# Optimization experiments

Hardware: AMD Instinct MI355X
Metric: run time of the kernel (lower is better)

Reference implementation:

```python
import jax, jax.numpy as jnp
import numpy as np

T_LATENCY = 2  # refractory latency (timesteps), from init_kwargs
FS_SCALE = 10.0  # FastSigmoid surrogate scale


@jax.custom_vjp
def fast_sigmoid_spike(u):
    return (u > 0).astype(u.dtype)

def _fs_fwd(u):
    return fast_sigmoid_spike(u), u

def _fs_bwd(u, g):
    return (g / (FS_SCALE * jnp.abs(u) + 1.0) ** 2,)

fast_sigmoid_spike.defvjp(_fs_fwd, _fs_bwd)


def setup_inputs() -> dict:
    key = jax.random.key(0)
    k1, k2, k3, k4 = jax.random.split(key, 4)
    B, N, T = 64, 1024, 512
    x = jax.random.normal(k1, (B, N, T), dtype=jnp.float32)
    beta = jax.random.uniform(k2, (N,), jnp.float32, 0.3, 0.95)   # leak
    p = jax.random.uniform(k3, (N,), jnp.float32, 0.5, 0.95)      # adaptation decay
    b = jax.random.uniform(k4, (N,), jnp.float32, 0.5, 1.5)       # adaptation strength
    return {"x": x, "beta": beta, "p": p, "b": b}


def reference(x, beta, p, b):
    # clamped effective params (matches torch @property accessors)
    beta_c = jnp.clip(beta, 0.001, 0.999)
    p_c = jnp.clip(jnp.abs(p), 0.0, 0.999)
    b_c = jnp.clip(jnp.abs(b), 0.001, 1.0)

    B, N, T = x.shape
    xt = jnp.moveaxis(x, 2, 0)  # [T, B, N]

    def step(carry, x_t):
        mem, spikes, refac, a, v_th = carry
        # spike-triggered refractory reset, then mask input during refractory window
        refac = jnp.where(spikes > 0, 0.0, refac)
        ic = jnp.where(refac < T_LATENCY, 0.0, x_t)
        refac = refac + 1.0
        # leaky integration
        new_mem = mem * beta_c + ic
        s = fast_sigmoid_spike(new_mem - v_th)
        # reset-by-subtraction-to-zero with detached spikes (detach_spike_grad=True)
        mem = new_mem * (1.0 - jax.lax.stop_gradient(s))
        # adaptive threshold
        a = p_c * a + s
        v_th = 1.0 + b_c * a
        return (mem, s, refac, a, v_th), s

    z = jnp.zeros((B, N), x.dtype)
    init = (z, z, jnp.full((B, N), float(T_LATENCY), x.dtype), z,
            jnp.ones((B, N), x.dtype))
    _, spikes_seq = jax.lax.scan(step, init, xt)  # [T, B, N]
    return jnp.moveaxis(spikes_seq, 0, 2)  # [B, N, T]
```

## Files before the change

kernel.cpp:

```cpp
#include <hip/hip_runtime.h>

#pragma clang fp contract(off)

#define ROWS    64
#define T_LEN   512
#define CHUNK   64
#define NCHUNK  (T_LEN / CHUNK)
#define NV      16
#define BUFW    (ROWS * CHUNK)
#define NPARAM  1024

typedef float f4_nt __attribute__((ext_vector_type(4)));

#define BARRIER() asm volatile("s_waitcnt lgkmcnt(0)\n\ts_barrier" ::: "memory")

#define GLOAD16(gp, lp)                                                \
    __builtin_amdgcn_global_load_lds(                                  \
        (const __attribute__((address_space(1))) void*)(gp),           \
        (__attribute__((address_space(3))) void*)(lp), 16, 0, 0)

__global__ __launch_bounds__(128) void snn_fwd(
    const float* __restrict__ x,
    const float* __restrict__ beta,
    const float* __restrict__ p,
    const float* __restrict__ bparam,
    float* __restrict__ out)
{
    __shared__ __align__(16) float inbuf[3][BUFW];
    __shared__ __align__(16) unsigned int bitlds[ROWS][16];

    const int tid     = threadIdx.x;
    const int wid     = tid >> 6;
    const int lane    = tid & 63;
    const int rowBase = blockIdx.x * ROWS;

    const float4* __restrict__ xv = (const float4*)x;
    float4* __restrict__ ov       = (float4*)out;

    const int t16 = lane & 15;
    const int r4  = lane >> 4;
    const int gEven = (rowBase + r4) * (T_LEN / 4) + (t16 ^ r4);
    const int gOdd  = gEven ^ 4;

    float mem = 0.0f, refac = 2.0f, a = 0.0f, vth = 1.0f, ps = 0.0f;
    float beta_c = 0.f, p_c = 0.f, b_c = 0.f;
    const int swl   = (lane & 3) | (((lane >> 2) & 1) << 2);
    const int cbase = lane * NV;

    if (wid == 0) {
        const int n = (rowBase + lane) & (NPARAM - 1);
        beta_c = fminf(fmaxf(beta[n], 0.001f), 0.999f);
        p_c    = fminf(fabsf(p[n]), 0.999f);
        b_c    = fminf(fmaxf(fabsf(bparam[n]), 0.001f), 1.0f);
    }

    unsigned int b0 = 0, b1 = 0;

    auto step = [&](float xt, unsigned int msk, unsigned int& bw) {
        refac = (ps > 0.0f) ? 0.0f : refac;
        const float ic = (refac < 2.0f) ? 0.0f : xt;
        refac += 1.0f;
        const float nm   = __fadd_rn(__fmul_rn(mem, beta_c), ic);
        const float diff = __fsub_rn(nm, vth);
        const bool  sp   = diff > 0.0f;
        const float s    = sp ? 1.0f : 0.0f;
        bw |= sp ? msk : 0u;
        mem = sp ? 0.0f : nm;
        a   = __fadd_rn(__fmul_rn(p_c, a), s);
        vth = __fadd_rn(1.0f, __fmul_rn(b_c, a));
        ps  = s;
    };

    auto issue = [&](int c, int buf) {
        float* lb = &inbuf[buf][0];
        #pragma unroll
        for (int it = 0; it < NV; ++it) {
            const int gidx = ((it & 1) ? gOdd : gEven)
                           + it * 4 * (T_LEN / 4) + c * NV;
            GLOAD16(&xv[gidx], lb + it * 256);
        }
    };

    if (wid == 1) {
        issue(0, 0);
        issue(1, 1);
        asm volatile("s_waitcnt vmcnt(16)" ::: "memory");
    }
    BARRIER();

    int km3 = 0;
    #pragma unroll 1
    for (int k = 0; k < NCHUNK; ++k) {
        if (wid == 0) {
            b0 = 0; b1 = 0;
            const float4* ib = (const float4*)inbuf[km3];
            #pragma unroll
            for (int g = 0; g < NV; ++g) {
                const float4 v = ib[cbase + (g ^ swl)];
                const int t = 4 * g;
                if (t < 32) {
                    step(v.x, 1u << (t + 0), b0);
                    step(v.y, 1u << (t + 1), b0);
                    step(v.z, 1u << (t + 2), b0);
                    step(v.w, 1u << (t + 3), b0);
                } else {
                    step(v.x, 1u << (t - 32), b1);
                    step(v.y, 1u << (t - 31), b1);
                    step(v.z, 1u << (t - 30), b1);
                    step(v.w, 1u << (t - 29), b1);
                }
            }
            *(uint2*)&bitlds[lane][2 * k] = make_uint2(b0, b1);
        } else {
            if (k + 2 < NCHUNK) {
                int nb = km3 + 2; if (nb >= 3) nb -= 3;
                issue(k + 2, nb);
            }
            if (k < NCHUNK - 2)
                asm volatile("s_waitcnt vmcnt(16)" ::: "memory");
            else if (k == NCHUNK - 2)
                asm volatile("s_waitcnt vmcnt(0)" ::: "memory");
        }
        BARRIER();
        ++km3; if (km3 == 3) km3 = 0;
    }

    const int obase = rowBase * (T_LEN / 4);
    #pragma unroll 4
    for (int i = 0; i < ROWS; ++i) {
        const unsigned int w = bitlds[i][tid >> 3];
        const int s = (tid & 7) * 4;
        float4 sv;
        sv.x = (float)((w >> (s + 0)) & 1u);
        sv.y = (float)((w >> (s + 1)) & 1u);
        sv.z = (float)((w >> (s + 2)) & 1u);
        sv.w = (float)((w >> (s + 3)) & 1u);
        __builtin_nontemporal_store(
            *reinterpret_cast<f4_nt*>(&sv),
            reinterpret_cast<f4_nt*>(&ov[obase + i * 128 + tid]));
    }
}

extern "C" void kernel_launch(void* const* d_in, const int* in_sizes, int n_in,
                              void* d_out, int out_size, void* d_ws, size_t ws_size,
                              hipStream_t stream) {
    const float* x    = (const float*)d_in[0];
    const float* beta = (const float*)d_in[1];
    const float* p    = (const float*)d_in[2];
    const float* b    = (const float*)d_in[3];
    float* out        = (float*)d_out;

    const int BN = 64 * 1024;
    snn_fwd<<<dim3(BN / ROWS), dim3(128), 0, stream>>>(x, beta, p, b, out);
}
```

Measured before the change: 244.9 us.

## Use tiny one-wave blocks loading whole rows, computing in LDS with 16 lanes

Replaces the 64-row block, which had a producer wave and a triple-buffered chunk pipeline, with 64-thread blocks that each handle 16 rows. Each block loads its full 16x512 slab into LDS at once with direct global-to-LDS loads, and 16 lanes run the serial recurrence while writing spikes back in place. The result is then stored out. The block count goes up by 4x, so latency is hidden through many resident blocks rather than explicit pipelining. Only 16 of 64 lanes do the serial compute, and the bit-packing step is dropped.

Result: slower. 279.2 us (+14.0%).

```diff
diff --git a/kernel.cpp b/kernel.cpp
--- a/kernel.cpp
+++ b/kernel.cpp
@@ -2,61 +2,51 @@
 
 #pragma clang fp contract(off)
 
-#define ROWS    64
+#define ROWSB   16
 #define T_LEN   512
-#define CHUNK   64
-#define NCHUNK  (T_LEN / CHUNK)
-#define NV      16
-#define BUFW    (ROWS * CHUNK)
+#define QPR     128
 #define NPARAM  1024
 
 typedef float f4_nt __attribute__((ext_vector_type(4)));
-
-#define BARRIER() asm volatile("s_waitcnt lgkmcnt(0)\n\ts_barrier" ::: "memory")
 
 #define GLOAD16(gp, lp)                                                \
     __builtin_amdgcn_global_load_lds(                                  \
         (const __attribute__((address_space(1))) void*)(gp),           \
         (__attribute__((address_space(3))) void*)(lp), 16, 0, 0)
 
-__global__ __launch_bounds__(128) void snn_fwd(
+__global__ __launch_bounds__(64) void snn_fwd(
     const float* __restrict__ x,
     const float* __restrict__ beta,
     const float* __restrict__ p,
     const float* __restrict__ bparam,
     float* __restrict__ out)
 {
-    __shared__ __align__(16) float inbuf[3][BUFW];
-    __shared__ __align__(16) unsigned int bitlds[ROWS][16];
+    __shared__ __align__(16) float4 xbuf[ROWSB * QPR];
 
-    const int tid     = threadIdx.x;
-    const int wid     = tid >> 6;
-    const int lane    = tid & 63;
-    const int rowBase = blockIdx.x * ROWS;
+    const int lane    = threadIdx.x;
+    const int rowBase = blockIdx.x * ROWSB;
 
-    const float4* __restrict__ xv = (const float4*)x;
-    float4* __restrict__ ov       = (float4*)out;
+    const float4* __restrict__ xq = (const float4*)x + (size_t)rowBase * QPR;
+    float4* __restrict__ oq       = (float4*)out + (size_t)rowBase * QPR;
 
-    const int t16 = lane & 15;
-    const int r4  = lane >> 4;
-    const int gEven = (rowBase + r4) * (T_LEN / 4) + (t16 ^ r4);
-    const int gOdd  = gEven ^ 4;
+    #pragma unroll
+    for (int j = 0; j < 2 * ROWSB; ++j) {
+        const int L  = j >> 1;
+        const int qg = (((j & 1) << 6) | lane) ^ (L & 7);
+        GLOAD16(xq + L * QPR + qg, (float*)xbuf + j * 256);
+    }
 
-    float mem = 0.0f, refac = 2.0f, a = 0.0f, vth = 1.0f, ps = 0.0f;
-    float beta_c = 0.f, p_c = 0.f, b_c = 0.f;
-    const int swl   = (lane & 3) | (((lane >> 2) & 1) << 2);
-    const int cbase = lane * NV;
-
-    if (wid == 0) {
-        const int n = (rowBase + lane) & (NPARAM - 1);
+    float beta_c, p_c, b_c;
+    {
+        const int n = (rowBase + (lane & (ROWSB - 1))) & (NPARAM - 1);
         beta_c = fminf(fmaxf(beta[n], 0.001f), 0.999f);
         p_c    = fminf(fabsf(p[n]), 0.999f);
         b_c    = fminf(fmaxf(fabsf(bparam[n]), 0.001f), 1.0f);
     }
 
-    unsigned int b0 = 0, b1 = 0;
+    float mem = 0.0f, refac = 2.0f, a = 0.0f, vth = 1.0f, ps = 0.0f;
 
-    auto step = [&](float xt, unsigned int msk, unsigned int& bw) {
+    auto step = [&](float xt) -> float {
         refac = (ps > 0.0f) ? 0.0f : refac;
         const float ic = (refac < 2.0f) ? 0.0f : xt;
         refac += 1.0f;
@@ -64,80 +54,42 @@
         const float diff = __fsub_rn(nm, vth);
         const bool  sp   = diff > 0.0f;
         const float s    = sp ? 1.0f : 0.0f;
-        bw |= sp ? msk : 0u;
         mem = sp ? 0.0f : nm;
         a   = __fadd_rn(__fmul_rn(p_c, a), s);
         vth = __fadd_rn(1.0f, __fmul_rn(b_c, a));
         ps  = s;
+        return s;
     };
 
-    auto issue = [&](int c, int buf) {
-        float* lb = &inbuf[buf][0];
-        #pragma unroll
-        for (int it = 0; it < NV; ++it) {
-            const int gidx = ((it & 1) ? gOdd : gEven)
-                           + it * 4 * (T_LEN / 4) + c * NV;
-            GLOAD16(&xv[gidx], lb + it * 256);
+    asm volatile("s_waitcnt vmcnt(0)" ::: "memory");
+
+    if (lane < ROWSB) {
+        const int L7 = lane & 7;
+        float4* xb = xbuf + lane * QPR;
+        float4 p0 = xb[0 ^ L7];
+        float4 p1 = xb[1 ^ L7];
+        #pragma unroll 2
+        for (int t4 = 0; t4 < QPR; t4 += 2) {
+            float4 n0 = xb[((t4 + 2) & (QPR - 1)) ^ L7];
+            float4 s0;
+            s0.x = step(p0.x); s0.y = step(p0.y);
+            s0.z = step(p0.z); s0.w = step(p0.w);
+            xb[t4 ^ L7] = s0;
+            float4 n1 = xb[((t4 + 3) & (QPR - 1)) ^ L7];
+            float4 s1;
+            s1.x = step(p1.x); s1.y = step(p1.y);
+            s1.z = step(p1.z); s1.w = step(p1.w);
+            xb[(t4 + 1) ^ L7] = s1;
+            p0 = n0; p1 = n1;
         }
-    };
-
-    if (wid == 1) {
-        issue(0, 0);
-        issue(1, 1);
-        asm volatile("s_waitcnt vmcnt(16)" ::: "memory");
-    }
-    BARRIER();
-
-    int km3 = 0;
-    #pragma unroll 1
-    for (int k = 0; k < NCHUNK; ++k) {
-        if (wid == 0) {
-            b0 = 0; b1 = 0;
-            const float4* ib = (const float4*)inbuf[km3];
-            #pragma unroll
-            for (int g = 0; g < NV; ++g) {
-                const float4 v = ib[cbase + (g ^ swl)];
-                const int t = 4 * g;
-                if (t < 32) {
-                    step(v.x, 1u << (t + 0), b0);
-                    step(v.y, 1u << (t + 1), b0);
-                    step(v.z, 1u << (t + 2), b0);
-                    step(v.w, 1u << (t + 3), b0);
-                } else {
-                    step(v.x, 1u << (t - 32), b1);
-                    step(v.y, 1u << (t - 31), b1);
-                    step(v.z, 1u << (t - 30), b1);
-                    step(v.w, 1u << (t - 29), b1);
-                }
-            }
-            *(uint2*)&bitlds[lane][2 * k] = make_uint2(b0, b1);
-        } else {
-            if (k + 2 < NCHUNK) {
-                int nb = km3 + 2; if (nb >= 3) nb -= 3;
-                issue(k + 2, nb);
-            }
-            if (k < NCHUNK - 2)
-                asm volatile("s_waitcnt vmcnt(16)" ::: "memory");
-            else if (k == NCHUNK - 2)
-                asm volatile("s_waitcnt vmcnt(0)" ::: "memory");
-        }
-        BARRIER();
-        ++km3; if (km3 == 3) km3 = 0;
     }
 
-    const int obase = rowBase * (T_LEN / 4);
-    #pragma unroll 4
-    for (int i = 0; i < ROWS; ++i) {
-        const unsigned int w = bitlds[i][tid >> 3];
-        const int s = (tid & 7) * 4;
-        float4 sv;
-        sv.x = (float)((w >> (s + 0)) & 1u);
-        sv.y = (float)((w >> (s + 1)) & 1u);
-        sv.z = (float)((w >> (s + 2)) & 1u);
-        sv.w = (float)((w >> (s + 3)) & 1u);
+    #pragma unroll
+    for (int j = 0; j < 2 * ROWSB; ++j) {
+        const float4 sv = xbuf[j * 64 + (lane ^ ((j >> 1) & 7))];
         __builtin_nontemporal_store(
-            *reinterpret_cast<f4_nt*>(&sv),
-            reinterpret_cast<f4_nt*>(&ov[obase + i * 128 + tid]));
+            *reinterpret_cast<const f4_nt*>(&sv),
+            reinterpret_cast<f4_nt*>(oq + j * 64 + lane));
     }
 }
 
@@ -151,5 +103,5 @@
     float* out        = (float*)d_out;
 
     const int BN = 64 * 1024;
-    snn_fwd<<<dim3(BN / ROWS), dim3(128), 0, stream>>>(x, beta, p, b, out);
+    snn_fwd<<<dim3(BN / ROWSB), dim3(64), 0, stream>>>(x, beta, p, b, out);
 }
```
